# Performance work log

Hardware: AMD Instinct MI355X
Metric: run time of the kernel (lower is better)

The kernel has to match this reference:

```python
import jax, jax.numpy as jnp
import numpy as np

B, I, H, M, A, R, S, O = 256, 512, 1024, 128, 2048, 4, 3, 512
RS = R * M                      # read_size = num_heads * memory_content_size
P_READ = M + S + 3              # key + shift + (beta, gate, gamma) per read head
P = R * P_READ + (3 * M + S + 3)  # write head adds erase(M) + add(M)


def setup_inputs() -> dict:
    key = jax.random.key(0)
    ks = jax.random.split(key, 16)
    x = jax.random.normal(ks[0], (B, I), dtype=jnp.float32)
    h_prev = 0.1 * jax.random.normal(ks[1], (B, H), dtype=jnp.float32)
    c_prev = 0.1 * jax.random.normal(ks[2], (B, H), dtype=jnp.float32)
    read_w_prev = jax.nn.softmax(jax.random.normal(ks[3], (B, R, A)), axis=-1)
    write_w_prev = jax.nn.softmax(jax.random.normal(ks[4], (B, A)), axis=-1)
    # init_state uses normal(mean=0.5, std=0.2) for memory
    memory_prev = 0.5 + 0.2 * jax.random.normal(ks[5], (B, M, A), dtype=jnp.float32)
    read_vec_prev = 0.1 * jax.random.normal(ks[6], (B, RS), dtype=jnp.float32)
    sc = 0.02
    Wx = sc * jax.random.normal(ks[7], (I + RS, 4 * H), dtype=jnp.float32)
    Wh = sc * jax.random.normal(ks[8], (H, 4 * H), dtype=jnp.float32)
    b_lstm = jnp.zeros((4 * H,), dtype=jnp.float32)
    Wo_h = sc * jax.random.normal(ks[9], (H, O), dtype=jnp.float32)
    bo_h = jnp.zeros((O,), dtype=jnp.float32)
    Wint = sc * jax.random.normal(ks[10], (H, P), dtype=jnp.float32)
    b_int = jnp.zeros((P,), dtype=jnp.float32)
    Wout = sc * jax.random.normal(ks[11], (RS, O), dtype=jnp.float32)
    b_out = jnp.zeros((O,), dtype=jnp.float32)
    return dict(x=x, h_prev=h_prev, c_prev=c_prev, read_w_prev=read_w_prev,
                write_w_prev=write_w_prev, memory_prev=memory_prev,
                read_vec_prev=read_vec_prev, Wx=Wx, Wh=Wh, b_lstm=b_lstm,
                Wo_h=Wo_h, bo_h=bo_h, Wint=Wint, b_int=b_int, Wout=Wout, b_out=b_out)


def _address(k, beta, g, s, gamma, w_prev, mem):
    """NTM/DNC addressing: cosine content sim -> softmax -> gate -> circular shift -> sharpen.
    k: [B,Rh,M], beta/g/gamma: [B,Rh], s: [B,Rh,S], w_prev: [B,Rh,A], mem: [B,M,A] -> w: [B,Rh,A]"""
    eps = 1e-8
    kn = jnp.linalg.norm(k, axis=-1, keepdims=True)          # [B,Rh,1]
    mn = jnp.linalg.norm(mem, axis=1)                        # [B,A]
    sim = jnp.einsum('brm,bma->bra', k, mem) / (kn * mn[:, None, :] + eps)
    w_c = jax.nn.softmax(beta[..., None] * sim, axis=-1)
    w_g = g[..., None] * w_c + (1.0 - g[..., None]) * w_prev
    # circular convolution over S shift offsets centered at 0
    rolled = jnp.stack([jnp.roll(w_g, off, axis=-1) for off in range(-(S // 2), S // 2 + 1)], axis=-1)  # [B,Rh,A,S]
    w_s = jnp.einsum('bras,brs->bra', rolled, s)
    w_pow = (w_s + 1e-12) ** gamma[..., None]
    return w_pow / (jnp.sum(w_pow, axis=-1, keepdims=True) + eps)


def reference(x, h_prev, c_prev, read_w_prev, write_w_prev, memory_prev, read_vec_prev,
              Wx, Wh, b_lstm, Wo_h, bo_h, Wint, b_int, Wout, b_out):
    b = x.shape[0]
    # ---- controller (LSTM over [input, prev read vector]) ----
    z = jnp.concatenate([x, read_vec_prev], axis=-1) @ Wx + h_prev @ Wh + b_lstm
    i_g, f_g, g_g, o_g = jnp.split(z, 4, axis=-1)
    c = jax.nn.sigmoid(f_g) * c_prev + jax.nn.sigmoid(i_g) * jnp.tanh(g_g)
    h = jax.nn.sigmoid(o_g) * jnp.tanh(c)
    output_from_hidden = h @ Wo_h + bo_h
    p = h @ Wint + b_int                                    # interface update_data
    # ---- read heads ----
    pr = p[:, :R * P_READ].reshape(b, R, P_READ)
    k_r = pr[..., :M]
    beta_r = jax.nn.softplus(pr[..., M])
    g_r = jax.nn.sigmoid(pr[..., M + 1])
    gamma_r = 1.0 + jax.nn.softplus(pr[..., M + 2])
    s_r = jax.nn.softmax(pr[..., M + 3:], axis=-1)
    w_read = _address(k_r, beta_r, g_r, s_r, gamma_r, read_w_prev, memory_prev)
    # ---- write head ----
    pw = p[:, R * P_READ:]
    k_w = pw[:, :M]
    beta_w = jax.nn.softplus(pw[:, M])
    g_w = jax.nn.sigmoid(pw[:, M + 1])
    gamma_w = 1.0 + jax.nn.softplus(pw[:, M + 2])
    s_w = jax.nn.softmax(pw[:, M + 3:M + 3 + S], axis=-1)
    erase = jax.nn.sigmoid(pw[:, M + 3 + S:2 * M + 3 + S])
    add = pw[:, 2 * M + 3 + S:]
    w_write = _address(k_w[:, None], beta_w[:, None], g_w[:, None], s_w[:, None],
                       gamma_w[:, None], write_w_prev[:, None], memory_prev)[:, 0]
    # ---- read from PREVIOUS memory (as in DNCCell.forward) ----
    read_vec = jnp.einsum('bma,bra->brm', memory_prev, w_read).reshape(b, RS)
    # ---- erase/add memory edit ----
    memory_new = memory_prev * (1.0 - jnp.einsum('bm,ba->bma', erase, w_write)) \
               + jnp.einsum('bm,ba->bma', add, w_write)
    final_output = output_from_hidden + read_vec @ Wout + b_out
    return final_output, memory_new
```

## Files before the change

### kernel.cpp

```cpp
#include <hip/hip_runtime.h>
#include <math.h>

#define B_ 256
#define I_ 512
#define H_ 1024
#define M_ 128
#define A_ 2048
#define R_ 4
#define S_ 3
#define O_ 512
#define RS_ 512
#define P_ 926
#define PW_OFF 536
#define NP_ 1438
#define SK_ 4

typedef unsigned short ushort_t;
typedef __attribute__((ext_vector_type(8))) short bf16x8;
typedef __attribute__((ext_vector_type(4))) float f32x4;
typedef __attribute__((ext_vector_type(4))) unsigned short u16x4;

__device__ __forceinline__ float sigmoidf_(float x) { return 1.0f / (1.0f + expf(-x)); }
__device__ __forceinline__ float softplusf_(float x) {
    return (x > 20.0f) ? x : log1pf(expf(x));
}
__device__ __forceinline__ ushort_t f2bf(float f) {
    unsigned int u = __float_as_uint(f);
    u = (u + 0x7FFFu + ((u >> 16) & 1u)) >> 16;
    return (ushort_t)u;
}

__device__ __forceinline__ float pval(const float* __restrict__ pp,
                                      const float* __restrict__ b_int,
                                      int b, int col) {
    size_t o = (size_t)b * NP_ + col;
    size_t st = (size_t)B_ * NP_;
    return b_int[col] + pp[o] + pp[o + st] + pp[o + 2 * st] + pp[o + 3 * st];
}

__device__ __forceinline__ float bsum8(float v, float* red, int wv, int l) {
    #pragma unroll
    for (int off = 32; off; off >>= 1) v += __shfl_down(v, off, 64);
    __syncthreads();
    if (l == 0) red[wv] = v;
    __syncthreads();
    return red[0] + red[1] + red[2] + red[3] + red[4] + red[5] + red[6] + red[7];
}
__device__ __forceinline__ float bmax8(float v, float* red, int wv, int l) {
    #pragma unroll
    for (int off = 32; off; off >>= 1) v = fmaxf(v, __shfl_down(v, off, 64));
    __syncthreads();
    if (l == 0) red[wv] = v;
    __syncthreads();
    float m0 = fmaxf(fmaxf(red[0], red[1]), fmaxf(red[2], red[3]));
    float m1 = fmaxf(fmaxf(red[4], red[5]), fmaxf(red[6], red[7]));
    return fmaxf(m0, m1);
}

__device__ __forceinline__ void transpose_tile(
    const float* __restrict__ W, ushort_t* __restrict__ WT,
    int K, int N, int ostride, int koff, int bx, int by, float (*tile)[33])
{
    int k0 = by * 32, n0 = bx * 32;
    int tx = threadIdx.x & 31, ty = threadIdx.x >> 5;
    #pragma unroll
    for (int i = 0; i < 4; ++i) {
        int k = ty + i * 8;
        int n = n0 + tx;
        float v = (n < N) ? W[(size_t)(k0 + k) * N + n] : 0.0f;
        tile[tx][k] = v;
    }
    __syncthreads();
    #pragma unroll
    for (int i = 0; i < 4; ++i) {
        int nl = ty + i * 8;
        int n = n0 + nl;
        if (n < N) WT[(size_t)n * ostride + koff + k0 + tx] = f2bf(tile[nl][tx]);
    }
}

__global__ __launch_bounds__(256) void setup_kernel(
    const float* __restrict__ x, const float* __restrict__ rv,
    const float* __restrict__ hp,
    const float* __restrict__ Wx, const float* __restrict__ Wh,
    const float* __restrict__ Wint, const float* __restrict__ Wo_h,
    ushort_t* __restrict__ xin, ushort_t* __restrict__ WxhT,
    ushort_t* __restrict__ WpT)
{
    __shared__ float tile[32][33];
    int r = blockIdx.x;
    if (r < 4096) { transpose_tile(Wx, WxhT, 1024, 4096, 2048, 0,    r % 128, r / 128, tile); return; }
    r -= 4096;
    if (r < 4096) { transpose_tile(Wh, WxhT, 1024, 4096, 2048, 1024, r % 128, r / 128, tile); return; }
    r -= 4096;
    if (r < 928)  { transpose_tile(Wint, WpT, 1024, 926, 1024, 0,    r % 29,  r / 29,  tile); return; }
    r -= 928;
    if (r < 512)  { transpose_tile(Wo_h, WpT + (size_t)926 * 1024, 1024, 512, 1024, 0, r % 16, r / 16, tile); return; }
    r -= 512;
    int idx = r * 256 + threadIdx.x;
    int b = idx >> 11, j = idx & 2047;
    float v;
    if (j < 512)       v = x[b * 512 + j];
    else if (j < 1024) v = rv[b * 512 + (j - 512)];
    else               v = hp[b * 1024 + (j - 1024)];
    xin[idx] = f2bf(v);
}

template<bool NALIGN>
__global__ __launch_bounds__(256) void gemm_bf16_k(
    const ushort_t* __restrict__ A, int lda,
    const ushort_t* __restrict__ BT, int ldb,
    float* __restrict__ Cpart,
    int N, int Ks)
{
    __shared__ ushort_t As[64][40];
    __shared__ ushort_t Bs[64][40];
    int tid = threadIdx.x;
    int bm0 = blockIdx.y * 64, bn0 = blockIdx.x * 64;
    int kbeg = blockIdx.z * Ks, kend = kbeg + Ks;
    int srow = tid >> 2;
    int scol = (tid & 3) << 3;
    int wv = tid >> 6, l = tid & 63;
    int wm = (wv & 1) * 32, wn = (wv >> 1) * 32;
    int lane16 = l & 15, quad = l >> 4;

    f32x4 z4 = {0.0f, 0.0f, 0.0f, 0.0f};
    f32x4 acc00 = z4, acc01 = z4, acc10 = z4, acc11 = z4;

    const ushort_t* ap = A + (size_t)(bm0 + srow) * lda + scol;
    bool bvalid = NALIGN || (bn0 + srow) < N;
    const ushort_t* bp = BT + (size_t)(bn0 + srow) * ldb + scol;
    float4 fz = {0.0f, 0.0f, 0.0f, 0.0f};

    for (int k0 = kbeg; k0 < kend; k0 += 32) {
        *(float4*)&As[srow][scol] = *(const float4*)(ap + k0);
        if (bvalid) *(float4*)&Bs[srow][scol] = *(const float4*)(bp + k0);
        else        *(float4*)&Bs[srow][scol] = fz;
        __syncthreads();
        bf16x8 a0 = *(const bf16x8*)&As[wm + lane16][quad * 8];
        bf16x8 a1 = *(const bf16x8*)&As[wm + 16 + lane16][quad * 8];
        bf16x8 b0 = *(const bf16x8*)&Bs[wn + lane16][quad * 8];
        bf16x8 b1 = *(const bf16x8*)&Bs[wn + 16 + lane16][quad * 8];
        acc00 = __builtin_amdgcn_mfma_f32_16x16x32_bf16(a0, b0, acc00, 0, 0, 0);
        acc01 = __builtin_amdgcn_mfma_f32_16x16x32_bf16(a0, b1, acc01, 0, 0, 0);
        acc10 = __builtin_amdgcn_mfma_f32_16x16x32_bf16(a1, b0, acc10, 0, 0, 0);
        acc11 = __builtin_amdgcn_mfma_f32_16x16x32_bf16(a1, b1, acc11, 0, 0, 0);
        __syncthreads();
    }

    float* C = Cpart + (size_t)blockIdx.z * gridDim.y * 64 * N;
    #pragma unroll
    for (int gi = 0; gi < 2; ++gi) {
        #pragma unroll
        for (int gj = 0; gj < 2; ++gj) {
            const f32x4& acc = gi == 0 ? (gj == 0 ? acc00 : acc01)
                                       : (gj == 0 ? acc10 : acc11);
            int col = bn0 + wn + gj * 16 + lane16;
            if (NALIGN || col < N) {
                #pragma unroll
                for (int r2 = 0; r2 < 4; ++r2) {
                    int row = bm0 + wm + gi * 16 + quad * 4 + r2;
                    C[(size_t)row * N + col] = acc[r2];
                }
            }
        }
    }
}

__global__ __launch_bounds__(256) void gates_kernel(
    const float* __restrict__ zpart, const float* __restrict__ b_lstm,
    const float* __restrict__ c_prev, ushort_t* __restrict__ h)
{
    int g = blockIdx.x * 256 + threadIdx.x;
    int b = g >> 8, j = (g & 255) << 2;
    size_t st = (size_t)B_ * 4096;
    size_t zb = (size_t)b * 4096 + j;
    f32x4 zs[4];
    #pragma unroll
    for (int q = 0; q < 4; ++q) {
        size_t o = zb + q * 1024;
        f32x4 v = *(const f32x4*)(zpart + o);
        v += *(const f32x4*)(zpart + o + st);
        v += *(const f32x4*)(zpart + o + 2 * st);
        v += *(const f32x4*)(zpart + o + 3 * st);
        v += *(const f32x4*)(b_lstm + q * 1024 + j);
        zs[q] = v;
    }
    f32x4 cp = *(const f32x4*)(c_prev + (size_t)b * 1024 + j);
    u16x4 hv;
    #pragma unroll
    for (int e = 0; e < 4; ++e) {
        float c = sigmoidf_(zs[1][e]) * cp[e] + sigmoidf_(zs[0][e]) * tanhf(zs[2][e]);
        hv[e] = f2bf(sigmoidf_(zs[3][e]) * tanhf(c));
    }
    *(u16x4*)(h + (size_t)b * 1024 + j) = hv;
}

__global__ __launch_bounds__(512) void mega_kernel(
    const float* __restrict__ mem, const float* __restrict__ pohpart,
    const float* __restrict__ b_int,
    const float* __restrict__ read_w_prev, const float* __restrict__ write_w_prev,
    const float* __restrict__ Wout, const float* __restrict__ bo_h,
    const float* __restrict__ b_out,
    float* __restrict__ out,
    float* __restrict__ mem_new)
{
    int b = blockIdx.x;
    int t = threadIdx.x;
    int wv = t >> 6, l = t & 63;

    __shared__ float dw[5][A_];
    __shared__ float wg[A_];
    __shared__ float ks[5][M_];
    __shared__ float rvp[M_][8][4];
    __shared__ float red[8];

    for (int idx = t; idx < 5 * M_; idx += 512) {
        int h = idx >> 7, m = idx & 127;
        int col = (h < 4) ? h * 134 + m : PW_OFF + m;
        ks[h][m] = pval(pohpart, b_int, b, col);
    }
    __syncthreads();

    const float* mb = mem + (size_t)b * M_ * A_ + 4 * t;
    f32x4 z = {0.0f, 0.0f, 0.0f, 0.0f};
    f32x4 d0 = z, d1 = z, d2 = z, d3 = z, d4 = z, nn = z;
    #pragma unroll 2
    for (int m = 0; m < M_; m += 4) {
        f32x4 vv[4];
        #pragma unroll
        for (int mm = 0; mm < 4; ++mm)
            vv[mm] = *(const f32x4*)(mb + (size_t)(m + mm) * A_);
        #pragma unroll
        for (int mm = 0; mm < 4; ++mm) {
            float k0 = ks[0][m + mm], k1 = ks[1][m + mm], k2 = ks[2][m + mm];
            float k3 = ks[3][m + mm], k4 = ks[4][m + mm];
            #pragma unroll
            for (int c = 0; c < 4; ++c) {
                float v = vv[mm][c];
                d0[c] += v * k0; d1[c] += v * k1; d2[c] += v * k2;
                d3[c] += v * k3; d4[c] += v * k4;
                nn[c] += v * v;
            }
        }
    }
    *(f32x4*)&dw[0][4 * t] = d0;
    *(f32x4*)&dw[1][4 * t] = d1;
    *(f32x4*)&dw[2][4 * t] = d2;
    *(f32x4*)&dw[3][4 * t] = d3;
    *(f32x4*)&dw[4][4 * t] = d4;
    f32x4 rt;
    #pragma unroll
    for (int c = 0; c < 4; ++c) rt[c] = sqrtf(nn[c]);

    for (int head = 0; head < 5; ++head) {
        int pb = (head < 4) ? head * 134 : PW_OFF;
        float beta  = softplusf_(pval(pohpart, b_int, b, pb + 128));
        float g     = sigmoidf_(pval(pohpart, b_int, b, pb + 129));
        float gamma = 1.0f + softplusf_(pval(pohpart, b_int, b, pb + 130));
        float e0 = pval(pohpart, b_int, b, pb + 131);
        float e1 = pval(pohpart, b_int, b, pb + 132);
        float e2 = pval(pohpart, b_int, b, pb + 133);
        float smax = fmaxf(e0, fmaxf(e1, e2));
        float x0 = __expf(e0 - smax), x1 = __expf(e1 - smax), x2 = __expf(e2 - smax);
        float sden = x0 + x1 + x2;
        float s0 = x0 / sden, s1 = x1 / sden, s2 = x2 / sden;

        float kacc = (t < M_) ? ks[head][t] * ks[head][t] : 0.0f;
        float kn = sqrtf(bsum8(kacc, red, wv, l));

        f32x4 dd = *(const f32x4*)&dw[head][4 * t];
        f32x4 lg;
        float lmax = -1e30f;
        #pragma unroll
        for (int c = 0; c < 4; ++c) {
            lg[c] = beta * dd[c] / (kn * rt[c] + 1e-8f);
            lmax = fmaxf(lmax, lg[c]);
        }
        lmax = bmax8(lmax, red, wv, l);
        f32x4 ex;
        float lsum = 0.0f;
        #pragma unroll
        for (int c = 0; c < 4; ++c) { ex[c] = __expf(lg[c] - lmax); lsum += ex[c]; }
        lsum = bsum8(lsum, red, wv, l);
        float inv_lsum = 1.0f / lsum;

        const float* wprev = (head < 4) ? read_w_prev + ((size_t)b * 4 + head) * A_
                                        : write_w_prev + (size_t)b * A_;
        f32x4 pv = *(const f32x4*)(wprev + 4 * t);
        f32x4 gv;
        #pragma unroll
        for (int c = 0; c < 4; ++c)
            gv[c] = g * (ex[c] * inv_lsum) + (1.0f - g) * pv[c];
        *(f32x4*)&wg[4 * t] = gv;
        __syncthreads();
        f32x4 wp;
        float psum = 0.0f;
        #pragma unroll
        for (int c = 0; c < 4; ++c) {
            int a = 4 * t + c;
            float ws = s0 * wg[(a + 1) & (A_ - 1)] + s1 * wg[a] + s2 * wg[(a + A_ - 1) & (A_ - 1)];
            wp[c] = __expf(gamma * __logf(ws + 1e-12f));
            psum += wp[c];
        }
        psum = bsum8(psum, red, wv, l);
        float inv = 1.0f / (psum + 1e-8f);
        #pragma unroll
        for (int c = 0; c < 4; ++c) wp[c] *= inv;
        *(f32x4*)&dw[head][4 * t] = wp;
        __syncthreads();
    }

    float* er_s = &ks[0][0];
    float* ad_s = &ks[1][0];
    if (t < M_)            er_s[t] = sigmoidf_(pval(pohpart, b_int, b, 670 + t));
    else if (t < 2 * M_)   ad_s[t - M_] = pval(pohpart, b_int, b, 798 + (t - M_));
    __syncthreads();

    f32x4 ww = *(const f32x4*)&dw[4][4 * t];
    f32x4 w0 = *(const f32x4*)&dw[0][4 * t];
    f32x4 w1 = *(const f32x4*)&dw[1][4 * t];
    f32x4 w2 = *(const f32x4*)&dw[2][4 * t];
    f32x4 w3 = *(const f32x4*)&dw[3][4 * t];
    const float* mrow = mem + (size_t)b * M_ * A_ + 4 * t;
    float* orow = mem_new + (size_t)b * M_ * A_ + 4 * t;
    #pragma unroll 1
    for (int m0v = 0; m0v < M_; m0v += 4) {
        f32x4 vv[4];
        #pragma unroll
        for (int mm = 0; mm < 4; ++mm)
            vv[mm] = *(const f32x4*)(mrow + (size_t)(m0v + mm) * A_);
        #pragma unroll
        for (int mm = 0; mm < 4; ++mm) {
            float er = er_s[m0v + mm], ad = ad_s[m0v + mm];
            f32x4 ov;
            float a0 = 0, a1 = 0, a2 = 0, a3 = 0;
            #pragma unroll
            for (int c = 0; c < 4; ++c) {
                float v = vv[mm][c];
                ov[c] = v * (1.0f - er * ww[c]) + ad * ww[c];
                a0 += v * w0[c]; a1 += v * w1[c]; a2 += v * w2[c]; a3 += v * w3[c];
            }
            *(f32x4*)(orow + (size_t)(m0v + mm) * A_) = ov;
            float ah0 = a0, ah1 = a1, ah2 = a2, ah3 = a3;
            #pragma unroll
            for (int off = 32; off; off >>= 1) {
                ah0 += __shfl_down(ah0, off, 64);
                ah1 += __shfl_down(ah1, off, 64);
                ah2 += __shfl_down(ah2, off, 64);
                ah3 += __shfl_down(ah3, off, 64);
            }
            if (l == 0) {
                rvp[m0v + mm][wv][0] = ah0;
                rvp[m0v + mm][wv][1] = ah1;
                rvp[m0v + mm][wv][2] = ah2;
                rvp[m0v + mm][wv][3] = ah3;
            }
        }
    }
    __syncthreads();

    float* rvs = wg;
    {
        int h = t >> 7, m = t & 127;
        float s = 0.0f;
        #pragma unroll
        for (int w8 = 0; w8 < 8; ++w8) s += rvp[m][w8][h];
        rvs[t] = s;
    }
    __syncthreads();

    float* part = &rvp[0][0][0];
    {
        int q = t >> 7;
        int oc = (t & 127) * 4;
        f32x4 acc = {0.0f, 0.0f, 0.0f, 0.0f};
        const float* wob = Wout + (size_t)q * M_ * O_ + oc;
        #pragma unroll 4
        for (int k = 0; k < M_; ++k) {
            float rvk = rvs[q * M_ + k];
            f32x4 wv4 = *(const f32x4*)(wob + (size_t)k * O_);
            #pragma unroll
            for (int c = 0; c < 4; ++c) acc[c] += rvk * wv4[c];
        }
        *(f32x4*)&part[q * 512 + oc] = acc;
    }
    __syncthreads();
    {
        int o = t;
        size_t st = (size_t)B_ * NP_;
        size_t po = (size_t)b * NP_ + 926 + o;
        float oh = pohpart[po] + pohpart[po + st] + pohpart[po + 2 * st] + pohpart[po + 3 * st];
        float s = part[o] + part[512 + o] + part[1024 + o] + part[1536 + o];
        out[(size_t)b * O_ + o] = s + oh + bo_h[o] + b_out[o];
    }
}

extern "C" void kernel_launch(void* const* d_in, const int* in_sizes, int n_in,
                              void* d_out, int out_size, void* d_ws, size_t ws_size,
                              hipStream_t stream) {
    (void)in_sizes; (void)n_in; (void)out_size; (void)ws_size;
    const float* x            = (const float*)d_in[0];
    const float* h_prev       = (const float*)d_in[1];
    const float* c_prev       = (const float*)d_in[2];
    const float* read_w_prev  = (const float*)d_in[3];
    const float* write_w_prev = (const float*)d_in[4];
    const float* memory_prev  = (const float*)d_in[5];
    const float* read_vec_prev= (const float*)d_in[6];
    const float* Wx           = (const float*)d_in[7];
    const float* Wh           = (const float*)d_in[8];
    const float* b_lstm       = (const float*)d_in[9];
    const float* Wo_h         = (const float*)d_in[10];
    const float* bo_h         = (const float*)d_in[11];
    const float* Wint         = (const float*)d_in[12];
    const float* b_int        = (const float*)d_in[13];
    const float* Wout         = (const float*)d_in[14];
    const float* b_out        = (const float*)d_in[15];
    float* out = (float*)d_out;
    float* mem_new_out = out + (size_t)B_ * O_;

    char* wsp = (char*)d_ws;
    ushort_t* xin_bf = (ushort_t*)wsp; wsp += (size_t)B_ * 2048 * 2;
    ushort_t* h_bf   = (ushort_t*)wsp; wsp += (size_t)B_ * H_ * 2;
    ushort_t* WxhT   = (ushort_t*)wsp; wsp += (size_t)4096 * 2048 * 2;
    ushort_t* WpT    = (ushort_t*)wsp; wsp += (size_t)NP_ * 1024 * 2;
    float* zpart     = (float*)wsp;    wsp += (size_t)SK_ * B_ * 4096 * 4;
    float* pohpart   = (float*)wsp;    wsp += (size_t)SK_ * B_ * NP_ * 4;

    setup_kernel<<<dim3(4096 + 4096 + 928 + 512 + 2048), 256, 0, stream>>>(
        x, read_vec_prev, h_prev, Wx, Wh, Wint, Wo_h,
        xin_bf, WxhT, WpT);
    gemm_bf16_k<true><<<dim3(4096 / 64, B_ / 64, SK_), 256, 0, stream>>>(
        xin_bf, 2048, WxhT, 2048, zpart, 4096, 2048 / SK_);
    gates_kernel<<<dim3(B_ * H_ / 1024), 256, 0, stream>>>(zpart, b_lstm, c_prev, h_bf);
    gemm_bf16_k<false><<<dim3(23, B_ / 64, SK_), 256, 0, stream>>>(
        h_bf, 1024, WpT, 1024, pohpart, NP_, 1024 / SK_);
    mega_kernel<<<dim3(B_), 512, 0, stream>>>(
        memory_prev, pohpart, b_int, read_w_prev, write_w_prev,
        Wout, bo_h, b_out, out, mem_new_out);
}
```

Measured before the change: 614.6 us.

## Split per-batch memory kernel across four cooperating blocks with global-flag sync

The single 512-thread block per batch row becomes four 256-thread blocks, each owning a quarter of the memory columns. Partial dot products, column norms and read-vector partials are exchanged through global workspace, with atomic-counter spin barriers between the blocks of a batch row. The addressing softmax and shift are computed redundantly by all four blocks, and the output projection is split by column. The goal is more blocks in flight to use the memory bandwidth better, at the cost of extra global traffic, redundant addressing work, and a risk of deadlock if sibling blocks are not co-resident.

```diff
diff --git a/kernel.cpp b/kernel.cpp
--- a/kernel.cpp
+++ b/kernel.cpp
@@ -18,6 +18,7 @@
 typedef unsigned short ushort_t;
 typedef __attribute__((ext_vector_type(8))) short bf16x8;
 typedef __attribute__((ext_vector_type(4))) float f32x4;
+typedef __attribute__((ext_vector_type(2))) float f32x2;
 typedef __attribute__((ext_vector_type(4))) unsigned short u16x4;
 
 __device__ __forceinline__ float sigmoidf_(float x) { return 1.0f / (1.0f + expf(-x)); }
@@ -38,23 +39,21 @@
     return b_int[col] + pp[o] + pp[o + st] + pp[o + 2 * st] + pp[o + 3 * st];
 }
 
-__device__ __forceinline__ float bsum8(float v, float* red, int wv, int l) {
+__device__ __forceinline__ float bsum4(float v, float* red, int wv, int l) {
     #pragma unroll
     for (int off = 32; off; off >>= 1) v += __shfl_down(v, off, 64);
     __syncthreads();
     if (l == 0) red[wv] = v;
     __syncthreads();
-    return red[0] + red[1] + red[2] + red[3] + red[4] + red[5] + red[6] + red[7];
-}
-__device__ __forceinline__ float bmax8(float v, float* red, int wv, int l) {
+    return red[0] + red[1] + red[2] + red[3];
+}
+__device__ __forceinline__ float bmax4(float v, float* red, int wv, int l) {
     #pragma unroll
     for (int off = 32; off; off >>= 1) v = fmaxf(v, __shfl_down(v, off, 64));
     __syncthreads();
     if (l == 0) red[wv] = v;
     __syncthreads();
-    float m0 = fmaxf(fmaxf(red[0], red[1]), fmaxf(red[2], red[3]));
-    float m1 = fmaxf(fmaxf(red[4], red[5]), fmaxf(red[6], red[7]));
-    return fmaxf(m0, m1);
+    return fmaxf(fmaxf(red[0], red[1]), fmaxf(red[2], red[3]));
 }
 
 __device__ __forceinline__ void transpose_tile(
@@ -85,7 +84,7 @@
     const float* __restrict__ Wx, const float* __restrict__ Wh,
     const float* __restrict__ Wint, const float* __restrict__ Wo_h,
     ushort_t* __restrict__ xin, ushort_t* __restrict__ WxhT,
-    ushort_t* __restrict__ WpT)
+    ushort_t* __restrict__ WpT, unsigned int* __restrict__ flags)
 {
     __shared__ float tile[32][33];
     int r = blockIdx.x;
@@ -97,13 +96,17 @@
     r -= 928;
     if (r < 512)  { transpose_tile(Wo_h, WpT + (size_t)926 * 1024, 1024, 512, 1024, 0, r % 16, r / 16, tile); return; }
     r -= 512;
-    int idx = r * 256 + threadIdx.x;
-    int b = idx >> 11, j = idx & 2047;
-    float v;
-    if (j < 512)       v = x[b * 512 + j];
-    else if (j < 1024) v = rv[b * 512 + (j - 512)];
-    else               v = hp[b * 1024 + (j - 1024)];
-    xin[idx] = f2bf(v);
+    if (r < 2048) {
+        int idx = r * 256 + threadIdx.x;
+        int b = idx >> 11, j = idx & 2047;
+        float v;
+        if (j < 512)       v = x[b * 512 + j];
+        else if (j < 1024) v = rv[b * 512 + (j - 512)];
+        else               v = hp[b * 1024 + (j - 1024)];
+        xin[idx] = f2bf(v);
+        return;
+    }
+    flags[threadIdx.x] = 0u;
 }
 
 template<bool NALIGN>
@@ -196,62 +199,80 @@
     *(u16x4*)(h + (size_t)b * 1024 + j) = hv;
 }
 
-__global__ __launch_bounds__(512) void mega_kernel(
+__global__ __launch_bounds__(256) void mega2_kernel(
     const float* __restrict__ mem, const float* __restrict__ pohpart,
     const float* __restrict__ b_int,
     const float* __restrict__ read_w_prev, const float* __restrict__ write_w_prev,
     const float* __restrict__ Wout, const float* __restrict__ bo_h,
     const float* __restrict__ b_out,
+    float* __restrict__ dots_g,
+    float* __restrict__ mn_g,
+    float* __restrict__ rvh_g,
+    unsigned int* __restrict__ flags,
     float* __restrict__ out,
     float* __restrict__ mem_new)
 {
-    int b = blockIdx.x;
+    int qb = blockIdx.x;
+    int b  = blockIdx.y;
     int t = threadIdx.x;
     int wv = t >> 6, l = t & 63;
 
-    __shared__ float dw[5][A_];
+    __shared__ float ks[5][M_];
+    __shared__ float w5[5][512];
     __shared__ float wg[A_];
-    __shared__ float ks[5][M_];
-    __shared__ float rvp[M_][8][4];
-    __shared__ float red[8];
-
-    for (int idx = t; idx < 5 * M_; idx += 512) {
+    __shared__ float rvp[M_][4][4];
+    __shared__ float red[4];
+
+    for (int idx = t; idx < 5 * M_; idx += 256) {
         int h = idx >> 7, m = idx & 127;
         int col = (h < 4) ? h * 134 + m : PW_OFF + m;
         ks[h][m] = pval(pohpart, b_int, b, col);
     }
     __syncthreads();
 
-    const float* mb = mem + (size_t)b * M_ * A_ + 4 * t;
-    f32x4 z = {0.0f, 0.0f, 0.0f, 0.0f};
-    f32x4 d0 = z, d1 = z, d2 = z, d3 = z, d4 = z, nn = z;
-    #pragma unroll 2
-    for (int m = 0; m < M_; m += 4) {
-        f32x4 vv[4];
-        #pragma unroll
-        for (int mm = 0; mm < 4; ++mm)
-            vv[mm] = *(const f32x4*)(mb + (size_t)(m + mm) * A_);
-        #pragma unroll
-        for (int mm = 0; mm < 4; ++mm) {
-            float k0 = ks[0][m + mm], k1 = ks[1][m + mm], k2 = ks[2][m + mm];
-            float k3 = ks[3][m + mm], k4 = ks[4][m + mm];
+    int a0 = qb * 512 + 2 * t;
+    {
+        const float* mb = mem + (size_t)b * M_ * A_ + a0;
+        f32x2 zz = {0.0f, 0.0f};
+        f32x2 d0 = zz, d1 = zz, d2 = zz, d3 = zz, d4 = zz, nn = zz;
+        for (int m = 0; m < M_; m += 8) {
+            f32x2 vv[8];
             #pragma unroll
-            for (int c = 0; c < 4; ++c) {
-                float v = vv[mm][c];
-                d0[c] += v * k0; d1[c] += v * k1; d2[c] += v * k2;
-                d3[c] += v * k3; d4[c] += v * k4;
-                nn[c] += v * v;
+            for (int j = 0; j < 8; ++j)
+                vv[j] = *(const f32x2*)(mb + (size_t)(m + j) * A_);
+            #pragma unroll
+            for (int j = 0; j < 8; ++j) {
+                float k0 = ks[0][m + j], k1 = ks[1][m + j], k2 = ks[2][m + j];
+                float k3 = ks[3][m + j], k4 = ks[4][m + j];
+                #pragma unroll
+                for (int c = 0; c < 2; ++c) {
+                    float v = vv[j][c];
+                    d0[c] += v * k0; d1[c] += v * k1; d2[c] += v * k2;
+                    d3[c] += v * k3; d4[c] += v * k4;
+                    nn[c] += v * v;
+                }
             }
         }
-    }
-    *(f32x4*)&dw[0][4 * t] = d0;
-    *(f32x4*)&dw[1][4 * t] = d1;
-    *(f32x4*)&dw[2][4 * t] = d2;
-    *(f32x4*)&dw[3][4 * t] = d3;
-    *(f32x4*)&dw[4][4 * t] = d4;
-    f32x4 rt;
-    #pragma unroll
-    for (int c = 0; c < 4; ++c) rt[c] = sqrtf(nn[c]);
+        size_t base = (size_t)b * 5 * A_ + a0;
+        *(f32x2*)(dots_g + base + 0 * A_) = d0;
+        *(f32x2*)(dots_g + base + 1 * A_) = d1;
+        *(f32x2*)(dots_g + base + 2 * A_) = d2;
+        *(f32x2*)(dots_g + base + 3 * A_) = d3;
+        *(f32x2*)(dots_g + base + 4 * A_) = d4;
+        f32x2 rt = {sqrtf(nn[0]), sqrtf(nn[1])};
+        *(f32x2*)(mn_g + (size_t)b * A_ + a0) = rt;
+    }
+    __threadfence();
+    __syncthreads();
+    if (t == 0) {
+        atomicAdd(&flags[b], 1u);
+        int guard = 0;
+        while (atomicAdd(&flags[b], 0u) < 4u && guard < (1 << 22)) {
+            __builtin_amdgcn_s_sleep(2); ++guard;
+        }
+    }
+    __syncthreads();
+    __threadfence();
 
     for (int head = 0; head < 5; ++head) {
         int pb = (head < 4) ? head * 134 : PW_OFF;
@@ -267,132 +288,159 @@
         float s0 = x0 / sden, s1 = x1 / sden, s2 = x2 / sden;
 
         float kacc = (t < M_) ? ks[head][t] * ks[head][t] : 0.0f;
-        float kn = sqrtf(bsum8(kacc, red, wv, l));
-
-        f32x4 dd = *(const f32x4*)&dw[head][4 * t];
-        f32x4 lg;
+        float kn = sqrtf(bsum4(kacc, red, wv, l));
+
+        const float* db = dots_g + ((size_t)b * 5 + head) * A_;
+        const float* mb = mn_g + (size_t)b * A_;
+        f32x4 dA = *(const f32x4*)(db + 4 * t);
+        f32x4 dB = *(const f32x4*)(db + 1024 + 4 * t);
+        f32x4 mA = *(const f32x4*)(mb + 4 * t);
+        f32x4 mB = *(const f32x4*)(mb + 1024 + 4 * t);
+        f32x4 lA, lB;
         float lmax = -1e30f;
         #pragma unroll
         for (int c = 0; c < 4; ++c) {
-            lg[c] = beta * dd[c] / (kn * rt[c] + 1e-8f);
-            lmax = fmaxf(lmax, lg[c]);
-        }
-        lmax = bmax8(lmax, red, wv, l);
-        f32x4 ex;
+            lA[c] = beta * dA[c] / (kn * mA[c] + 1e-8f);
+            lB[c] = beta * dB[c] / (kn * mB[c] + 1e-8f);
+            lmax = fmaxf(lmax, fmaxf(lA[c], lB[c]));
+        }
+        lmax = bmax4(lmax, red, wv, l);
+        f32x4 eA, eB;
         float lsum = 0.0f;
         #pragma unroll
-        for (int c = 0; c < 4; ++c) { ex[c] = __expf(lg[c] - lmax); lsum += ex[c]; }
-        lsum = bsum8(lsum, red, wv, l);
+        for (int c = 0; c < 4; ++c) {
+            eA[c] = __expf(lA[c] - lmax);
+            eB[c] = __expf(lB[c] - lmax);
+            lsum += eA[c] + eB[c];
+        }
+        lsum = bsum4(lsum, red, wv, l);
         float inv_lsum = 1.0f / lsum;
 
         const float* wprev = (head < 4) ? read_w_prev + ((size_t)b * 4 + head) * A_
                                         : write_w_prev + (size_t)b * A_;
-        f32x4 pv = *(const f32x4*)(wprev + 4 * t);
-        f32x4 gv;
-        #pragma unroll
-        for (int c = 0; c < 4; ++c)
-            gv[c] = g * (ex[c] * inv_lsum) + (1.0f - g) * pv[c];
-        *(f32x4*)&wg[4 * t] = gv;
+        f32x4 pA = *(const f32x4*)(wprev + 4 * t);
+        f32x4 pB = *(const f32x4*)(wprev + 1024 + 4 * t);
+        f32x4 gA, gB;
+        #pragma unroll
+        for (int c = 0; c < 4; ++c) {
+            gA[c] = g * (eA[c] * inv_lsum) + (1.0f - g) * pA[c];
+            gB[c] = g * (eB[c] * inv_lsum) + (1.0f - g) * pB[c];
+        }
+        *(f32x4*)&wg[4 * t] = gA;
+        *(f32x4*)&wg[1024 + 4 * t] = gB;
         __syncthreads();
-        f32x4 wp;
+        f32x4 wA, wB;
         float psum = 0.0f;
         #pragma unroll
         for (int c = 0; c < 4; ++c) {
             int a = 4 * t + c;
             float ws = s0 * wg[(a + 1) & (A_ - 1)] + s1 * wg[a] + s2 * wg[(a + A_ - 1) & (A_ - 1)];
-            wp[c] = __expf(gamma * __logf(ws + 1e-12f));
-            psum += wp[c];
-        }
-        psum = bsum8(psum, red, wv, l);
+            wA[c] = __expf(gamma * __logf(ws + 1e-12f));
+            a = 1024 + 4 * t + c;
+            ws = s0 * wg[(a + 1) & (A_ - 1)] + s1 * wg[a] + s2 * wg[(a + A_ - 1) & (A_ - 1)];
+            wB[c] = __expf(gamma * __logf(ws + 1e-12f));
+            psum += wA[c] + wB[c];
+        }
+        psum = bsum4(psum, red, wv, l);
         float inv = 1.0f / (psum + 1e-8f);
         #pragma unroll
-        for (int c = 0; c < 4; ++c) wp[c] *= inv;
-        *(f32x4*)&dw[head][4 * t] = wp;
-        __syncthreads();
-    }
-
-    float* er_s = &ks[0][0];
-    float* ad_s = &ks[1][0];
-    if (t < M_)            er_s[t] = sigmoidf_(pval(pohpart, b_int, b, 670 + t));
-    else if (t < 2 * M_)   ad_s[t - M_] = pval(pohpart, b_int, b, 798 + (t - M_));
-    __syncthreads();
-
-    f32x4 ww = *(const f32x4*)&dw[4][4 * t];
-    f32x4 w0 = *(const f32x4*)&dw[0][4 * t];
-    f32x4 w1 = *(const f32x4*)&dw[1][4 * t];
-    f32x4 w2 = *(const f32x4*)&dw[2][4 * t];
-    f32x4 w3 = *(const f32x4*)&dw[3][4 * t];
-    const float* mrow = mem + (size_t)b * M_ * A_ + 4 * t;
-    float* orow = mem_new + (size_t)b * M_ * A_ + 4 * t;
-    #pragma unroll 1
-    for (int m0v = 0; m0v < M_; m0v += 4) {
-        f32x4 vv[4];
-        #pragma unroll
-        for (int mm = 0; mm < 4; ++mm)
-            vv[mm] = *(const f32x4*)(mrow + (size_t)(m0v + mm) * A_);
-        #pragma unroll
-        for (int mm = 0; mm < 4; ++mm) {
-            float er = er_s[m0v + mm], ad = ad_s[m0v + mm];
-            f32x4 ov;
-            float a0 = 0, a1 = 0, a2 = 0, a3 = 0;
+        for (int c = 0; c < 4; ++c) { wA[c] *= inv; wB[c] *= inv; }
+        if ((t >> 7) == qb)
+            *(f32x4*)&w5[head][4 * t - qb * 512] = wA;
+        if ((t >> 7) == qb - 2)
+            *(f32x4*)&w5[head][1024 + 4 * t - qb * 512] = wB;
+    }
+    if (t < M_)  ks[0][t] = sigmoidf_(pval(pohpart, b_int, b, 670 + t));
+    else         ks[1][t - M_] = pval(pohpart, b_int, b, 798 + (t - M_));
+    __syncthreads();
+
+    {
+        int lc = 2 * t;
+        f32x2 ww = *(const f32x2*)&w5[4][lc];
+        f32x2 w0 = *(const f32x2*)&w5[0][lc];
+        f32x2 w1 = *(const f32x2*)&w5[1][lc];
+        f32x2 w2 = *(const f32x2*)&w5[2][lc];
+        f32x2 w3 = *(const f32x2*)&w5[3][lc];
+        const float* mrow = mem + (size_t)b * M_ * A_ + a0;
+        float* orow = mem_new + (size_t)b * M_ * A_ + a0;
+        for (int m = 0; m < M_; m += 8) {
+            f32x2 vv[8];
             #pragma unroll
-            for (int c = 0; c < 4; ++c) {
-                float v = vv[mm][c];
-                ov[c] = v * (1.0f - er * ww[c]) + ad * ww[c];
-                a0 += v * w0[c]; a1 += v * w1[c]; a2 += v * w2[c]; a3 += v * w3[c];
+            for (int j = 0; j < 8; ++j)
+                vv[j] = *(const f32x2*)(mrow + (size_t)(m + j) * A_);
+            #pragma unroll
+            for (int j = 0; j < 8; ++j) {
+                float er = ks[0][m + j], ad = ks[1][m + j];
+                f32x2 ov;
+                float s0a = 0, s1a = 0, s2a = 0, s3a = 0;
+                #pragma unroll
+                for (int c = 0; c < 2; ++c) {
+                    float v = vv[j][c];
+                    ov[c] = v * (1.0f - er * ww[c]) + ad * ww[c];
+                    s0a += v * w0[c]; s1a += v * w1[c];
+                    s2a += v * w2[c]; s3a += v * w3[c];
+                }
+                *(f32x2*)(orow + (size_t)(m + j) * A_) = ov;
+                #pragma unroll
+                for (int off = 32; off; off >>= 1) {
+                    s0a += __shfl_down(s0a, off, 64);
+                    s1a += __shfl_down(s1a, off, 64);
+                    s2a += __shfl_down(s2a, off, 64);
+                    s3a += __shfl_down(s3a, off, 64);
+                }
+                if (l == 0) {
+                    rvp[m + j][wv][0] = s0a; rvp[m + j][wv][1] = s1a;
+                    rvp[m + j][wv][2] = s2a; rvp[m + j][wv][3] = s3a;
+                }
             }
-            *(f32x4*)(orow + (size_t)(m0v + mm) * A_) = ov;
-            float ah0 = a0, ah1 = a1, ah2 = a2, ah3 = a3;
-            #pragma unroll
-            for (int off = 32; off; off >>= 1) {
-                ah0 += __shfl_down(ah0, off, 64);
-                ah1 += __shfl_down(ah1, off, 64);
-                ah2 += __shfl_down(ah2, off, 64);
-                ah3 += __shfl_down(ah3, off, 64);
-            }
-            if (l == 0) {
-                rvp[m0v + mm][wv][0] = ah0;
-                rvp[m0v + mm][wv][1] = ah1;
-                rvp[m0v + mm][wv][2] = ah2;
-                rvp[m0v + mm][wv][3] = ah3;
-            }
-        }
-    }
-    __syncthreads();
-
-    float* rvs = wg;
-    {
-        int h = t >> 7, m = t & 127;
-        float s = 0.0f;
-        #pragma unroll
-        for (int w8 = 0; w8 < 8; ++w8) s += rvp[m][w8][h];
-        rvs[t] = s;
+        }
+    }
+    __syncthreads();
+    for (int idx = t; idx < RS_; idx += 256) {
+        int m = idx & 127, r = idx >> 7;
+        float s = rvp[m][0][r] + rvp[m][1][r] + rvp[m][2][r] + rvp[m][3][r];
+        rvh_g[((size_t)qb * B_ + b) * RS_ + r * M_ + m] = s;
+    }
+    __threadfence();
+    __syncthreads();
+    if (t == 0) {
+        atomicAdd(&flags[b], 1u);
+        int guard = 0;
+        while (atomicAdd(&flags[b], 0u) < 8u && guard < (1 << 22)) {
+            __builtin_amdgcn_s_sleep(2); ++guard;
+        }
+    }
+    __syncthreads();
+    __threadfence();
+
+    for (int k = t; k < RS_; k += 256) {
+        float s = rvh_g[(size_t)b * RS_ + k]
+                + rvh_g[((size_t)B_ + b) * RS_ + k]
+                + rvh_g[((size_t)2 * B_ + b) * RS_ + k]
+                + rvh_g[((size_t)3 * B_ + b) * RS_ + k];
+        wg[k] = s;
     }
     __syncthreads();
 
     float* part = &rvp[0][0][0];
     {
-        int q = t >> 7;
-        int oc = (t & 127) * 4;
-        f32x4 acc = {0.0f, 0.0f, 0.0f, 0.0f};
-        const float* wob = Wout + (size_t)q * M_ * O_ + oc;
+        int kq = t >> 7;
+        int oc = t & 127;
+        int col = qb * 128 + oc;
+        float acc = 0.0f;
+        const float* wob = Wout + (size_t)kq * 256 * O_ + col;
         #pragma unroll 4
-        for (int k = 0; k < M_; ++k) {
-            float rvk = rvs[q * M_ + k];
-            f32x4 wv4 = *(const f32x4*)(wob + (size_t)k * O_);
-            #pragma unroll
-            for (int c = 0; c < 4; ++c) acc[c] += rvk * wv4[c];
-        }
-        *(f32x4*)&part[q * 512 + oc] = acc;
-    }
-    __syncthreads();
-    {
-        int o = t;
+        for (int k = 0; k < 256; ++k)
+            acc += wg[kq * 256 + k] * wob[(size_t)k * O_];
+        part[t] = acc;
+    }
+    __syncthreads();
+    if (t < 128) {
+        int col = qb * 128 + t;
         size_t st = (size_t)B_ * NP_;
-        size_t po = (size_t)b * NP_ + 926 + o;
+        size_t po = (size_t)b * NP_ + 926 + col;
         float oh = pohpart[po] + pohpart[po + st] + pohpart[po + 2 * st] + pohpart[po + 3 * st];
-        float s = part[o] + part[512 + o] + part[1024 + o] + part[1536 + o];
-        out[(size_t)b * O_ + o] = s + oh + bo_h[o] + b_out[o];
+        out[(size_t)b * O_ + col] = part[t] + part[t + 128] + oh + bo_h[col] + b_out[col];
     }
 }
 
@@ -426,16 +474,20 @@
     ushort_t* WpT    = (ushort_t*)wsp; wsp += (size_t)NP_ * 1024 * 2;
     float* zpart     = (float*)wsp;    wsp += (size_t)SK_ * B_ * 4096 * 4;
     float* pohpart   = (float*)wsp;    wsp += (size_t)SK_ * B_ * NP_ * 4;
-
-    setup_kernel<<<dim3(4096 + 4096 + 928 + 512 + 2048), 256, 0, stream>>>(
+    float* dots_g    = (float*)wsp;    wsp += (size_t)B_ * 5 * A_ * 4;
+    float* mn_g      = (float*)wsp;    wsp += (size_t)B_ * A_ * 4;
+    float* rvh_g     = (float*)wsp;    wsp += (size_t)4 * B_ * RS_ * 4;
+    unsigned int* flags = (unsigned int*)wsp; wsp += (size_t)B_ * 4;
+
+    setup_kernel<<<dim3(4096 + 4096 + 928 + 512 + 2048 + 1), 256, 0, stream>>>(
         x, read_vec_prev, h_prev, Wx, Wh, Wint, Wo_h,
-        xin_bf, WxhT, WpT);
+        xin_bf, WxhT, WpT, flags);
     gemm_bf16_k<true><<<dim3(4096 / 64, B_ / 64, SK_), 256, 0, stream>>>(
         xin_bf, 2048, WxhT, 2048, zpart, 4096, 2048 / SK_);
     gates_kernel<<<dim3(B_ * H_ / 1024), 256, 0, stream>>>(zpart, b_lstm, c_prev, h_bf);
     gemm_bf16_k<false><<<dim3(23, B_ / 64, SK_), 256, 0, stream>>>(
         h_bf, 1024, WpT, 1024, pohpart, NP_, 1024 / SK_);
-    mega_kernel<<<dim3(B_), 512, 0, stream>>>(
+    mega2_kernel<<<dim3(4, B_), 256, 0, stream>>>(
         memory_prev, pohpart, b_int, read_w_prev, write_w_prev,
-        Wout, bo_h, b_out, out, mem_new_out);
-}
+        Wout, bo_h, b_out, dots_g, mn_g, rvh_g, flags, out, mem_new_out);
+}
```

Measured after the change: 1.249 ms. 2.03x slower.
